# Kernel optimization log

Hardware: AMD Instinct MI355X
Metric: run time of the kernel (lower is better)

## Reference

```python
import jax, jax.numpy as jnp
import numpy as np


def setup_inputs() -> dict:
    key = jax.random.key(0)
    kq, kk, kv = jax.random.split(key, 3)
    B, H, S, D = 2, 16, 2048, 64
    Q = jax.random.normal(kq, (B, H, S, D), dtype=jnp.float32)
    K = jax.random.normal(kk, (B, H, S, D), dtype=jnp.float32)
    V = jax.random.normal(kv, (B, H, S, D), dtype=jnp.float32)
    return {"Q": Q, "K": K, "V": V}


def reference(Q, K, V):
    # Faithful to the torch module: NO 1/sqrt(d_k) scaling (d_k is computed
    # but never used in the original forward).
    scores = jnp.einsum('bhqd,bhkd->bhqk', Q, K)      # [B,H,S,S]
    attn = jax.nn.softmax(scores, axis=-1)
    out = jnp.einsum('bhqk,bhkd->bhqd', attn, V)      # [B,H,S,D]
    return out
```

## Files before the change

### kernel.cpp

```cpp
#include <hip/hip_runtime.h>


typedef __bf16    bf16_t;
typedef _Float16  f16_t;
typedef __bf16    bf16x8 __attribute__((ext_vector_type(8)));
typedef _Float16  f16x8  __attribute__((ext_vector_type(8)));
typedef float     f32x4  __attribute__((ext_vector_type(4)));

constexpr int S  = 2048;
constexpr int Dh = 64;
constexpr int KT = 64;
constexpr int QT = 128;

__device__ __forceinline__ int sw(int row, int col) {
    return row * 64 + ((((col >> 3) ^ (row & 7)) << 3) | (col & 7));
}

template<bool SPLIT>
__global__ __launch_bounds__(256, 4)
void attn_kernel(const float* __restrict__ Qg,
                 const float* __restrict__ Kg,
                 const float* __restrict__ Vg,
                 float* __restrict__ Og,
                 float* __restrict__ Opart,
                 float* __restrict__ lpart)
{
    __shared__ f16_t  Khs[KT * Dh];
    __shared__ bf16_t Vts[Dh * KT];
    __shared__ bf16_t Pbs[QT * Dh];

    const int tid  = threadIdx.x;
    const int lane = tid & 63;
    const int wv   = tid >> 6;
    const int l15  = lane & 15;
    const int qd   = lane >> 4;
    const int wb   = wv * 32;

    const int bx   = blockIdx.x;
    const int head = bx & 31;
    const int r5   = bx >> 5;
    const int qt   = SPLIT ? (r5 >> 1) : r5;
    const int half = SPLIT ? (r5 & 1) : 0;
    const int tile = head * 16 + qt;
    const int ch0  = SPLIT ? half * 16 : 0;
    const int nch  = SPLIT ? 16 : 32;

    const float* Qp = Qg + (size_t)tile * QT * Dh;
    const float* Kp = Kg + (size_t)head * S * Dh;
    const float* Vp = Vg + (size_t)head * S * Dh;

    const int skey = tid >> 4;
    const int sc4  = (tid & 15) * 4;
    const int vkb  = (tid >> 4) * 4;
    const int vc4  = (tid & 15) * 4;

    f16x8 qf[2][2];
    #pragma unroll
    for (int sub = 0; sub < 2; ++sub) {
        const float* qrow = Qp + (size_t)(wb + sub * 16 + l15) * Dh;
        #pragma unroll
        for (int ks = 0; ks < 2; ++ks) {
            const float* p = qrow + ks * 32 + qd * 8;
            const float4 a = *(const float4*)(p);
            const float4 b = *(const float4*)(p + 4);
            const float xs[8] = {a.x, a.y, a.z, a.w, b.x, b.y, b.z, b.w};
            #pragma unroll
            for (int j = 0; j < 8; ++j) qf[sub][ks][j] = (f16_t)xs[j];
        }
    }

    f32x4 oa[2][4];
    float lp[2];
    #pragma unroll
    for (int s2 = 0; s2 < 2; ++s2) {
        lp[s2] = 0.f;
        #pragma unroll
        for (int t = 0; t < 4; ++t) oa[s2][t] = (f32x4){0.f, 0.f, 0.f, 0.f};
    }

    float4 kbuf[4], vbuf[4];
    {
        const float* Kc = Kp + (size_t)ch0 * KT * Dh;
        const float* Vc = Vp + (size_t)ch0 * KT * Dh;
        #pragma unroll
        for (int it = 0; it < 4; ++it)
            kbuf[it] = *(const float4*)(Kc + (size_t)(it * 16 + skey) * Dh + sc4);
        #pragma unroll
        for (int i = 0; i < 4; ++i)
            vbuf[i] = *(const float4*)(Vc + (size_t)(vkb + i) * Dh + vc4);
    }

    #pragma unroll 1
    for (int ci = 0; ci < nch; ++ci) {
        __syncthreads();

        #pragma unroll
        for (int it = 0; it < 4; ++it) {
            const float xs[4] = {kbuf[it].x, kbuf[it].y, kbuf[it].z, kbuf[it].w};
            union { f16_t h[4]; uint2 u; } ph;
            #pragma unroll
            for (int j = 0; j < 4; ++j) ph.h[j] = (f16_t)xs[j];
            *(uint2*)&Khs[sw(it * 16 + skey, sc4)] = ph.u;
        }
        {
            const float rs[4][4] = {{vbuf[0].x, vbuf[1].x, vbuf[2].x, vbuf[3].x},
                                    {vbuf[0].y, vbuf[1].y, vbuf[2].y, vbuf[3].y},
                                    {vbuf[0].z, vbuf[1].z, vbuf[2].z, vbuf[3].z},
                                    {vbuf[0].w, vbuf[1].w, vbuf[2].w, vbuf[3].w}};
            #pragma unroll
            for (int i = 0; i < 4; ++i) {
                union { bf16_t h[4]; uint2 u; } pv;
                #pragma unroll
                for (int j = 0; j < 4; ++j) pv.h[j] = (bf16_t)rs[i][j];
                *(uint2*)&Vts[sw(vc4 + i, vkb)] = pv.u;
            }
        }
        __syncthreads();

        if (ci + 1 < nch) {
            const float* Kc = Kp + (size_t)(ch0 + ci + 1) * KT * Dh;
            const float* Vc = Vp + (size_t)(ch0 + ci + 1) * KT * Dh;
            #pragma unroll
            for (int it = 0; it < 4; ++it)
                kbuf[it] = *(const float4*)(Kc + (size_t)(it * 16 + skey) * Dh + sc4);
            #pragma unroll
            for (int i = 0; i < 4; ++i)
                vbuf[i] = *(const float4*)(Vc + (size_t)(vkb + i) * Dh + vc4);
        }

        #pragma unroll
        for (int np = 0; np < 2; ++np) {
            f32x4 st[2][2];
            #pragma unroll
            for (int s2 = 0; s2 < 2; ++s2)
                #pragma unroll
                for (int t = 0; t < 2; ++t) st[s2][t] = (f32x4){0.f, 0.f, 0.f, 0.f};
            #pragma unroll
            for (int ks = 0; ks < 2; ++ks) {
                const int co = ks * 32 + qd * 8;
                const f16x8 ak0 = *(const f16x8*)&Khs[sw((np * 2 + 0) * 16 + l15, co)];
                const f16x8 ak1 = *(const f16x8*)&Khs[sw((np * 2 + 1) * 16 + l15, co)];
                #pragma unroll
                for (int s2 = 0; s2 < 2; ++s2) {
                    st[s2][0] = __builtin_amdgcn_mfma_f32_16x16x32_f16(ak0, qf[s2][ks], st[s2][0], 0, 0, 0);
                    st[s2][1] = __builtin_amdgcn_mfma_f32_16x16x32_f16(ak1, qf[s2][ks], st[s2][1], 0, 0, 0);
                }
            }
            #pragma unroll
            for (int s2 = 0; s2 < 2; ++s2) {
                #pragma unroll
                for (int t = 0; t < 2; ++t) {
                    union { bf16_t h[4]; uint2 u; } pb;
                    #pragma unroll
                    for (int r = 0; r < 4; ++r) {
                        const bf16_t b = (bf16_t)__expf(st[s2][t][r]);
                        lp[s2] += (float)b;
                        pb.h[r] = b;
                    }
                    *(uint2*)&Pbs[sw(wb + s2 * 16 + l15, (np * 2 + t) * 16 + qd * 4)] = pb.u;
                }
            }
        }

        #pragma unroll
        for (int ks = 0; ks < 2; ++ks) {
            const int co = ks * 32 + qd * 8;
            const bf16x8 pa0 = *(const bf16x8*)&Pbs[sw(wb + l15,      co)];
            const bf16x8 pa1 = *(const bf16x8*)&Pbs[sw(wb + 16 + l15, co)];
            #pragma unroll
            for (int dt = 0; dt < 4; ++dt) {
                const bf16x8 vb = *(const bf16x8*)&Vts[sw(dt * 16 + l15, co)];
                oa[0][dt] = __builtin_amdgcn_mfma_f32_16x16x32_bf16(pa0, vb, oa[0][dt], 0, 0, 0);
                oa[1][dt] = __builtin_amdgcn_mfma_f32_16x16x32_bf16(pa1, vb, oa[1][dt], 0, 0, 0);
            }
        }
    }

    #pragma unroll
    for (int s2 = 0; s2 < 2; ++s2) {
        lp[s2] += __shfl_xor(lp[s2], 16, 64);
        lp[s2] += __shfl_xor(lp[s2], 32, 64);
    }

    if (SPLIT) {
        float* Po = Opart + (size_t)(tile * 2 + half) * (QT * Dh);
        float* lq = lpart + (size_t)(tile * 2 + half) * QT;
        #pragma unroll
        for (int s2 = 0; s2 < 2; ++s2) {
            if (qd == 0) lq[wb + s2 * 16 + l15] = lp[s2];
            #pragma unroll
            for (int r = 0; r < 4; ++r) {
                const int row = wb + s2 * 16 + qd * 4 + r;
                #pragma unroll
                for (int dt = 0; dt < 4; ++dt)
                    Po[(size_t)row * Dh + dt * 16 + l15] = oa[s2][dt][r];
            }
        }
    } else {
        float* Op = Og + (size_t)tile * QT * Dh;
        #pragma unroll
        for (int s2 = 0; s2 < 2; ++s2) {
            #pragma unroll
            for (int r = 0; r < 4; ++r) {
                const float inv = 1.0f / __shfl(lp[s2], qd * 4 + r, 64);
                const int row = wb + s2 * 16 + qd * 4 + r;
                #pragma unroll
                for (int dt = 0; dt < 4; ++dt)
                    Op[(size_t)row * Dh + dt * 16 + l15] = oa[s2][dt][r] * inv;
            }
        }
    }
}

__global__ __launch_bounds__(256)
void combine_kernel(const float* __restrict__ Opart,
                    const float* __restrict__ lpart,
                    float* __restrict__ Og)
{
    const int i  = blockIdx.x * 256 + threadIdx.x;
    const int q  = i >> 11;
    const int rw = (i >> 4) & 127;
    const size_t e = (size_t)(i & 2047) * 4;
    const float4 a = *(const float4*)(Opart + (size_t)(2 * q)     * (QT * Dh) + e);
    const float4 b = *(const float4*)(Opart + (size_t)(2 * q + 1) * (QT * Dh) + e);
    const float  l = lpart[(size_t)(2 * q) * QT + rw] + lpart[(size_t)(2 * q + 1) * QT + rw];
    const float inv = 1.0f / l;
    float4 o;
    o.x = (a.x + b.x) * inv;
    o.y = (a.y + b.y) * inv;
    o.z = (a.z + b.z) * inv;
    o.w = (a.w + b.w) * inv;
    *(float4*)(Og + (size_t)i * 4) = o;
}

extern "C" void kernel_launch(void* const* d_in, const int* in_sizes, int n_in,
                              void* d_out, int out_size, void* d_ws, size_t ws_size,
                              hipStream_t stream)
{
    const float* Q = (const float*)d_in[0];
    const float* K = (const float*)d_in[1];
    const float* V = (const float*)d_in[2];
    float*       O = (float*)d_out;

    constexpr size_t NPART       = 1024;
    constexpr size_t OPART_ELEMS = NPART * QT * Dh;
    constexpr size_t LPART_ELEMS = NPART * QT;
    constexpr size_t NEED = (OPART_ELEMS + LPART_ELEMS) * sizeof(float);

    if (ws_size >= NEED) {
        float* Opart = (float*)d_ws;
        float* lpart = Opart + OPART_ELEMS;
        attn_kernel<true><<<dim3(1024), dim3(256), 0, stream>>>(
            Q, K, V, nullptr, Opart, lpart);
        const int n4 = (int)(OPART_ELEMS / 2 / 4);
        combine_kernel<<<dim3(n4 / 256), dim3(256), 0, stream>>>(Opart, lpart, O);
    } else {
        attn_kernel<false><<<dim3(512), dim3(256), 0, stream>>>(
            Q, K, V, O, nullptr, nullptr);
    }
}
```

Before: 154.3 us.

## Pre-convert K/V to swizzled half precision in a prep kernel, use exp2

Adds a prep kernel that converts K to f16 and V to transposed bf16 once, stored in the workspace already in the swizzled shared-memory layout. The attention kernel then does straight 16-byte copies into LDS instead of reconverting K/V in every block, and each block moves half the global bytes for K/V. Q is pre-scaled by log2(e) so the kernel can call exp2 directly, and setprio brackets raise wave priority around the MFMA sections. The cost is an extra kernel launch and a larger workspace requirement, and the fast path only runs when the workspace is big enough.

```diff
diff --git a/kernel.cpp b/kernel.cpp
--- a/kernel.cpp
+++ b/kernel.cpp
@@ -11,23 +11,65 @@
 constexpr int Dh = 64;
 constexpr int KT = 64;
 constexpr int QT = 128;
+constexpr float LOG2E = 1.44269504088896340736f;
 
 __device__ __forceinline__ int sw(int row, int col) {
     return row * 64 + ((((col >> 3) ^ (row & 7)) << 3) | (col & 7));
 }
 
-template<bool SPLIT>
+__global__ __launch_bounds__(256)
+void prep_kernel(const float* __restrict__ Kg, const float* __restrict__ Vg,
+                 f16_t* __restrict__ Kpre, bf16_t* __restrict__ Vpre)
+{
+    const int tid = threadIdx.x;
+    const int hc  = blockIdx.x;
+    const float* Kc = Kg + (size_t)hc * (KT * Dh);
+    const float* Vc = Vg + (size_t)hc * (KT * Dh);
+    f16_t*  Ko = Kpre + (size_t)hc * (KT * Dh);
+    bf16_t* Vo = Vpre + (size_t)hc * (KT * Dh);
+
+    const int skey = tid >> 4;
+    const int sc4  = (tid & 15) * 4;
+    #pragma unroll
+    for (int it = 0; it < 4; ++it) {
+        const float4 k4 = *(const float4*)(Kc + (size_t)(it * 16 + skey) * Dh + sc4);
+        const float xs[4] = {k4.x, k4.y, k4.z, k4.w};
+        union { f16_t h[4]; uint2 u; } ph;
+        #pragma unroll
+        for (int j = 0; j < 4; ++j) ph.h[j] = (f16_t)xs[j];
+        *(uint2*)&Ko[sw(it * 16 + skey, sc4)] = ph.u;
+    }
+    const int vkb = (tid >> 4) * 4;
+    const int vc4 = (tid & 15) * 4;
+    float4 vb4[4];
+    #pragma unroll
+    for (int i = 0; i < 4; ++i)
+        vb4[i] = *(const float4*)(Vc + (size_t)(vkb + i) * Dh + vc4);
+    const float rs[4][4] = {{vb4[0].x, vb4[1].x, vb4[2].x, vb4[3].x},
+                            {vb4[0].y, vb4[1].y, vb4[2].y, vb4[3].y},
+                            {vb4[0].z, vb4[1].z, vb4[2].z, vb4[3].z},
+                            {vb4[0].w, vb4[1].w, vb4[2].w, vb4[3].w}};
+    #pragma unroll
+    for (int i = 0; i < 4; ++i) {
+        union { bf16_t h[4]; uint2 u; } pv;
+        #pragma unroll
+        for (int j = 0; j < 4; ++j) pv.h[j] = (bf16_t)rs[i][j];
+        *(uint2*)&Vo[sw(vc4 + i, vkb)] = pv.u;
+    }
+}
+
+template<bool SPLIT, bool PRE>
 __global__ __launch_bounds__(256, 4)
 void attn_kernel(const float* __restrict__ Qg,
-                 const float* __restrict__ Kg,
-                 const float* __restrict__ Vg,
+                 const void* __restrict__ Kin,
+                 const void* __restrict__ Vin,
                  float* __restrict__ Og,
                  float* __restrict__ Opart,
                  float* __restrict__ lpart)
 {
-    __shared__ f16_t  Khs[KT * Dh];
-    __shared__ bf16_t Vts[Dh * KT];
-    __shared__ bf16_t Pbs[QT * Dh];
+    __shared__ alignas(16) f16_t  Khs[KT * Dh];
+    __shared__ alignas(16) bf16_t Vts[Dh * KT];
+    __shared__ alignas(16) bf16_t Pbs[QT * Dh];
 
     const int tid  = threadIdx.x;
     const int lane = tid & 63;
@@ -46,8 +88,6 @@
     const int nch  = SPLIT ? 16 : 32;
 
     const float* Qp = Qg + (size_t)tile * QT * Dh;
-    const float* Kp = Kg + (size_t)head * S * Dh;
-    const float* Vp = Vg + (size_t)head * S * Dh;
 
     const int skey = tid >> 4;
     const int sc4  = (tid & 15) * 4;
@@ -65,7 +105,7 @@
             const float4 b = *(const float4*)(p + 4);
             const float xs[8] = {a.x, a.y, a.z, a.w, b.x, b.y, b.z, b.w};
             #pragma unroll
-            for (int j = 0; j < 8; ++j) qf[sub][ks][j] = (f16_t)xs[j];
+            for (int j = 0; j < 8; ++j) qf[sub][ks][j] = (f16_t)(xs[j] * LOG2E);
         }
     }
 
@@ -78,10 +118,16 @@
         for (int t = 0; t < 4; ++t) oa[s2][t] = (f32x4){0.f, 0.f, 0.f, 0.f};
     }
 
+    uint4  pk[2], pv[2];
     float4 kbuf[4], vbuf[4];
-    {
-        const float* Kc = Kp + (size_t)ch0 * KT * Dh;
-        const float* Vc = Vp + (size_t)ch0 * KT * Dh;
+    if constexpr (PRE) {
+        const uint4* Kc = (const uint4*)Kin + (size_t)(head * 32 + ch0) * 512;
+        const uint4* Vc = (const uint4*)Vin + (size_t)(head * 32 + ch0) * 512;
+        pk[0] = Kc[tid]; pk[1] = Kc[tid + 256];
+        pv[0] = Vc[tid]; pv[1] = Vc[tid + 256];
+    } else {
+        const float* Kc = (const float*)Kin + (size_t)(head * 32 + ch0) * (KT * Dh);
+        const float* Vc = (const float*)Vin + (size_t)(head * 32 + ch0) * (KT * Dh);
         #pragma unroll
         for (int it = 0; it < 4; ++it)
             kbuf[it] = *(const float4*)(Kc + (size_t)(it * 16 + skey) * Dh + sc4);
@@ -94,38 +140,48 @@
     for (int ci = 0; ci < nch; ++ci) {
         __syncthreads();
 
-        #pragma unroll
-        for (int it = 0; it < 4; ++it) {
-            const float xs[4] = {kbuf[it].x, kbuf[it].y, kbuf[it].z, kbuf[it].w};
-            union { f16_t h[4]; uint2 u; } ph;
-            #pragma unroll
-            for (int j = 0; j < 4; ++j) ph.h[j] = (f16_t)xs[j];
-            *(uint2*)&Khs[sw(it * 16 + skey, sc4)] = ph.u;
-        }
-        {
+        if constexpr (PRE) {
+            ((uint4*)Khs)[tid] = pk[0]; ((uint4*)Khs)[tid + 256] = pk[1];
+            ((uint4*)Vts)[tid] = pv[0]; ((uint4*)Vts)[tid + 256] = pv[1];
+        } else {
+            #pragma unroll
+            for (int it = 0; it < 4; ++it) {
+                const float xs[4] = {kbuf[it].x, kbuf[it].y, kbuf[it].z, kbuf[it].w};
+                union { f16_t h[4]; uint2 u; } ph;
+                #pragma unroll
+                for (int j = 0; j < 4; ++j) ph.h[j] = (f16_t)xs[j];
+                *(uint2*)&Khs[sw(it * 16 + skey, sc4)] = ph.u;
+            }
             const float rs[4][4] = {{vbuf[0].x, vbuf[1].x, vbuf[2].x, vbuf[3].x},
                                     {vbuf[0].y, vbuf[1].y, vbuf[2].y, vbuf[3].y},
                                     {vbuf[0].z, vbuf[1].z, vbuf[2].z, vbuf[3].z},
                                     {vbuf[0].w, vbuf[1].w, vbuf[2].w, vbuf[3].w}};
             #pragma unroll
             for (int i = 0; i < 4; ++i) {
-                union { bf16_t h[4]; uint2 u; } pv;
-                #pragma unroll
-                for (int j = 0; j < 4; ++j) pv.h[j] = (bf16_t)rs[i][j];
-                *(uint2*)&Vts[sw(vc4 + i, vkb)] = pv.u;
+                union { bf16_t h[4]; uint2 u; } pvv;
+                #pragma unroll
+                for (int j = 0; j < 4; ++j) pvv.h[j] = (bf16_t)rs[i][j];
+                *(uint2*)&Vts[sw(vc4 + i, vkb)] = pvv.u;
             }
         }
         __syncthreads();
 
         if (ci + 1 < nch) {
-            const float* Kc = Kp + (size_t)(ch0 + ci + 1) * KT * Dh;
-            const float* Vc = Vp + (size_t)(ch0 + ci + 1) * KT * Dh;
-            #pragma unroll
-            for (int it = 0; it < 4; ++it)
-                kbuf[it] = *(const float4*)(Kc + (size_t)(it * 16 + skey) * Dh + sc4);
-            #pragma unroll
-            for (int i = 0; i < 4; ++i)
-                vbuf[i] = *(const float4*)(Vc + (size_t)(vkb + i) * Dh + vc4);
+            if constexpr (PRE) {
+                const uint4* Kc = (const uint4*)Kin + (size_t)(head * 32 + ch0 + ci + 1) * 512;
+                const uint4* Vc = (const uint4*)Vin + (size_t)(head * 32 + ch0 + ci + 1) * 512;
+                pk[0] = Kc[tid]; pk[1] = Kc[tid + 256];
+                pv[0] = Vc[tid]; pv[1] = Vc[tid + 256];
+            } else {
+                const float* Kc = (const float*)Kin + (size_t)(head * 32 + ch0 + ci + 1) * (KT * Dh);
+                const float* Vc = (const float*)Vin + (size_t)(head * 32 + ch0 + ci + 1) * (KT * Dh);
+                #pragma unroll
+                for (int it = 0; it < 4; ++it)
+                    kbuf[it] = *(const float4*)(Kc + (size_t)(it * 16 + skey) * Dh + sc4);
+                #pragma unroll
+                for (int i = 0; i < 4; ++i)
+                    vbuf[i] = *(const float4*)(Vc + (size_t)(vkb + i) * Dh + vc4);
+            }
         }
 
         #pragma unroll
@@ -135,6 +191,7 @@
             for (int s2 = 0; s2 < 2; ++s2)
                 #pragma unroll
                 for (int t = 0; t < 2; ++t) st[s2][t] = (f32x4){0.f, 0.f, 0.f, 0.f};
+            __builtin_amdgcn_s_setprio(1);
             #pragma unroll
             for (int ks = 0; ks < 2; ++ks) {
                 const int co = ks * 32 + qd * 8;
@@ -146,6 +203,7 @@
                     st[s2][1] = __builtin_amdgcn_mfma_f32_16x16x32_f16(ak1, qf[s2][ks], st[s2][1], 0, 0, 0);
                 }
             }
+            __builtin_amdgcn_s_setprio(0);
             #pragma unroll
             for (int s2 = 0; s2 < 2; ++s2) {
                 #pragma unroll
@@ -153,15 +211,16 @@
                     union { bf16_t h[4]; uint2 u; } pb;
                     #pragma unroll
                     for (int r = 0; r < 4; ++r) {
-                        const bf16_t b = (bf16_t)__expf(st[s2][t][r]);
-                        lp[s2] += (float)b;
-                        pb.h[r] = b;
+                        const float e = __builtin_amdgcn_exp2f(st[s2][t][r]);
+                        lp[s2] += e;
+                        pb.h[r] = (bf16_t)e;
                     }
                     *(uint2*)&Pbs[sw(wb + s2 * 16 + l15, (np * 2 + t) * 16 + qd * 4)] = pb.u;
                 }
             }
         }
 
+        __builtin_amdgcn_s_setprio(1);
         #pragma unroll
         for (int ks = 0; ks < 2; ++ks) {
             const int co = ks * 32 + qd * 8;
@@ -174,6 +233,7 @@
                 oa[1][dt] = __builtin_amdgcn_mfma_f32_16x16x32_bf16(pa1, vb, oa[1][dt], 0, 0, 0);
             }
         }
+        __builtin_amdgcn_s_setprio(0);
     }
 
     #pragma unroll
@@ -245,17 +305,36 @@
     constexpr size_t NPART       = 1024;
     constexpr size_t OPART_ELEMS = NPART * QT * Dh;
     constexpr size_t LPART_ELEMS = NPART * QT;
-    constexpr size_t NEED = (OPART_ELEMS + LPART_ELEMS) * sizeof(float);
-
-    if (ws_size >= NEED) {
+    constexpr size_t KVPRE_ELEMS = 32ull * S * Dh;
+    constexpr size_t OP_BYTES    = OPART_ELEMS * sizeof(float);
+    constexpr size_t LP_BYTES    = LPART_ELEMS * sizeof(float);
+    constexpr size_t KV_BYTES    = 2 * KVPRE_ELEMS * 2;
+
+    const int n4 = (int)(OPART_ELEMS / 2 / 4);
+
+    if (ws_size >= OP_BYTES + LP_BYTES + KV_BYTES) {
+        float*  Opart = (float*)d_ws;
+        float*  lpart = Opart + OPART_ELEMS;
+        f16_t*  Kpre  = (f16_t*)(lpart + LPART_ELEMS);
+        bf16_t* Vpre  = (bf16_t*)(Kpre + KVPRE_ELEMS);
+        prep_kernel<<<dim3(1024), dim3(256), 0, stream>>>(K, V, Kpre, Vpre);
+        attn_kernel<true, true><<<dim3(1024), dim3(256), 0, stream>>>(
+            Q, Kpre, Vpre, nullptr, Opart, lpart);
+        combine_kernel<<<dim3(n4 / 256), dim3(256), 0, stream>>>(Opart, lpart, O);
+    } else if (ws_size >= OP_BYTES + LP_BYTES) {
         float* Opart = (float*)d_ws;
         float* lpart = Opart + OPART_ELEMS;
-        attn_kernel<true><<<dim3(1024), dim3(256), 0, stream>>>(
+        attn_kernel<true, false><<<dim3(1024), dim3(256), 0, stream>>>(
             Q, K, V, nullptr, Opart, lpart);
-        const int n4 = (int)(OPART_ELEMS / 2 / 4);
         combine_kernel<<<dim3(n4 / 256), dim3(256), 0, stream>>>(Opart, lpart, O);
+    } else if (ws_size >= KV_BYTES) {
+        f16_t*  Kpre = (f16_t*)d_ws;
+        bf16_t* Vpre = (bf16_t*)(Kpre + KVPRE_ELEMS);
+        prep_kernel<<<dim3(1024), dim3(256), 0, stream>>>(K, V, Kpre, Vpre);
+        attn_kernel<false, true><<<dim3(512), dim3(256), 0, stream>>>(
+            Q, Kpre, Vpre, O, nullptr, nullptr);
     } else {
-        attn_kernel<false><<<dim3(512), dim3(256), 0, stream>>>(
+        attn_kernel<false, false><<<dim3(512), dim3(256), 0, stream>>>(
             Q, K, V, O, nullptr, nullptr);
     }
 }
```

Result: slower. 179.4 us (+16.3%).
